# Optimization experiments

Measured on AMD Instinct MI355X. Metric: run time of the kernel, lower is better.

The kernel has to match this reference:

```python
import jax, jax.numpy as jnp
from jax import lax
import numpy as np

B, T, N, D = 16, 2048, 8, 512


def _div_term(d):
    # exp(arange(0,d,2) * -(ln 10000)/d), as in FixedEmbedding
    return jnp.exp(jnp.arange(0, d, 2).astype(jnp.float32) * (-np.log(10000.0) / d))


def _fixed_table(c, d):
    pos = jnp.arange(c, dtype=jnp.float32)[:, None]
    ang = pos * _div_term(d)  # [c, d/2]
    tab = jnp.zeros((c, d), dtype=jnp.float32)
    tab = tab.at[:, 0::2].set(jnp.sin(ang)).at[:, 1::2].set(jnp.cos(ang))
    return tab


def setup_inputs() -> dict:
    key = jax.random.key(0)
    k1, k2, k3 = jax.random.split(key, 3)
    x = jax.random.normal(k1, (B, T, N), dtype=jnp.float32)
    x_mark = jax.random.randint(k2, (B, T, 4), 0, 7).astype(jnp.int64)
    conv_w = jax.random.normal(k3, (D, N, 3), dtype=jnp.float32) * 0.05
    return {"x": x, "x_mark": x_mark, "conv_w": conv_w}


def reference(x, x_mark, conv_w):
    b, t, n = x.shape
    d = conv_w.shape[0]

    # --- TokenEmbedding: Conv1d(c_in->d_model, k=3, circular padding, no bias) ---
    xp = jnp.transpose(x, (0, 2, 1))  # [b, n, t]
    xpad = jnp.concatenate([xp[..., -1:], xp, xp[..., :1]], axis=-1)  # circular pad 1
    val = lax.conv_general_dilated(
        xpad, conv_w, window_strides=(1,), padding="VALID",
        dimension_numbers=("NCH", "OIH", "NCH"))  # [b, d, t]
    val = jnp.transpose(val, (0, 2, 1))  # [b, t, d]

    # --- TemporalEmbedding (fixed sinusoidal tables), freq='h' ---
    # columns: 0=month(<13), 1=day(<32), 2=weekday(<7), 3=hour(<24)
    temp = (_fixed_table(24, d)[x_mark[:, :, 3]]
            + _fixed_table(7, d)[x_mark[:, :, 2]]
            + _fixed_table(32, d)[x_mark[:, :, 1]]
            + _fixed_table(13, d)[x_mark[:, :, 0]])  # [b, t, d]

    # --- Cycle_PositionalEmbedding (k=1) ---
    fft_abs = jnp.abs(jnp.fft.rfft(x, axis=1))  # [b, t//2+1, n]
    top_idx = jnp.argmax(fft_abs, axis=1)  # [b, n]; topk(k=1) == argmax (first max)
    freqs = jnp.fft.fftfreq(t, d=1.0)  # length t; rfft indices are in range
    periods = jnp.clip(t / freqs[top_idx], 1.0, float(t))  # [b, n]; 0-freq -> inf -> t
    time_idx = jnp.arange(t, dtype=jnp.float32)[None, :, None]  # [1, t, 1]
    pidx = jnp.floor(time_idx % periods[:, None, :])  # [b, t, n] (.long() truncation)

    # FixedEmbedding row for index p is sin/cos(p*div) independent of c_in
    ang = pidx[..., None] * _div_term(d)  # [b, t, n, d/2]
    pe = jnp.stack([jnp.sin(ang), jnp.cos(ang)], axis=-1).reshape(b, t, n, d)
    cyc = pe.mean(axis=2)  # [b, t, d]

    # dropout is identity in eval mode
    return val + temp + cyc
```

## Files before the change

### kernel.cpp

```cpp
#include <hip/hip_runtime.h>
#include <math.h>

#define B_ 16
#define T_ 2048
#define N_ 8
#define D_ 512
#define DTW 4
#define LPAD 520

#define NEG_W0 (-3.0679615757712823e-3f)
#define NEG_W32 (-0.19634954084936207f)
#define NEG_W1024 (-6.1359231515425647e-3f)
#define NEG_LDIV (-0.035977892078031555f)

typedef __attribute__((ext_vector_type(8))) short bf16x8;
typedef __attribute__((ext_vector_type(4))) float f32x4;

static __device__ __forceinline__ short f2bf(float f) {
  unsigned int u = __float_as_uint(f);
  unsigned int r = u + 0x7FFFu + ((u >> 16) & 1u);
  return (short)(r >> 16);
}


__global__ __launch_bounds__(1024) void prep_kernel(
    const float* __restrict__ x, const int* __restrict__ xmark,
    const float* __restrict__ convw, float* __restrict__ pmax,
    float* __restrict__ nyqS, float* __restrict__ tab,
    short* __restrict__ amat, short* __restrict__ xbf,
    short* __restrict__ cnt) {
  int tid = threadIdx.x;
  int blk = blockIdx.x;

  if (blk >= 256) {
    int j = blk - 256;
    if (j < 32) {
      int r = j * 1024 + tid;
      const float4* xr = (const float4*)(x + (size_t)r * 8);
      float4 lo = xr[0], hi = xr[1];
      bf16x8 v;
      v[0] = f2bf(lo.x); v[1] = f2bf(lo.y); v[2] = f2bf(lo.z); v[3] = f2bf(lo.w);
      v[4] = f2bf(hi.x); v[5] = f2bf(hi.y); v[6] = f2bf(hi.z); v[7] = f2bf(hi.w);
      *(bf16x8*)(xbf + (size_t)r * 8) = v;
      int4 mk = *(const int4*)(xmark + (size_t)r * 4);
      bf16x8 cv;
#pragma unroll
      for (int p = 0; p < 8; ++p) {
        int cc = (mk.x == p) + (mk.y == p) + (mk.z == p) + (mk.w == p);
        cv[p] = f2bf((float)cc);
      }
      *(bf16x8*)(cnt + (size_t)r * 8) = cv;
    } else if (j == 32) {
      if (tid < 512) {
        int d = tid;
        short row[32];
#pragma unroll
        for (int kk = 0; kk < 24; ++kk) {
          int g = kk >> 3, n = kk & 7;
          row[kk] = f2bf(convw[d * 24 + n * 3 + g]);
        }
        float divv = expf((float)(d >> 1) * NEG_LDIV);
        float s1, c1;
        sincosf(divv, &s1, &c1);
        int odd = d & 1;
        row[24] = f2bf(odd ? 1.f : 0.f);
        float ps = s1, pc = c1;
        row[25] = f2bf(odd ? pc : ps);
#pragma unroll
        for (int p = 2; p < 7; ++p) {
          float ns = fmaf(ps, c1, pc * s1);
          float nc = fmaf(pc, c1, -ps * s1);
          ps = ns; pc = nc;
          row[24 + p] = f2bf(odd ? pc : ps);
        }
        row[31] = 0;
#pragma unroll
        for (int q = 0; q < 4; ++q)
          *(bf16x8*)(amat + d * 32 + q * 8) = *(bf16x8*)&row[q * 8];
      }
    } else {
      int gt = (j - 33) * 1024 + tid;
      int tb = gt >> 7;
      int d4 = gt & 127;
      float dv0 = expf((float)(d4 * 2) * NEG_LDIV);
      float dv1 = expf((float)(d4 * 2 + 1) * NEG_LDIV);
      float tf = (float)(tb * 16);
      float s0, c0, s1, c1, r0s, r0c, r1s, r1c;
      sincosf(tf * dv0, &s0, &c0);
      sincosf(tf * dv1, &s1, &c1);
      sincosf(dv0, &r0s, &r0c);
      sincosf(dv1, &r1s, &r1c);
      float* row = tab + (size_t)(tb * 16) * D_ + d4 * 4;
#pragma unroll
      for (int u = 0; u < 16; ++u) {
        f32x4 v; v[0] = s0; v[1] = c0; v[2] = s1; v[3] = c1;
        *(f32x4*)row = v;
        row += D_;
        float ns0 = fmaf(s0, r0c, c0 * r0s), nc0 = fmaf(c0, r0c, -s0 * r0s);
        s0 = ns0; c0 = nc0;
        float ns1 = fmaf(s1, r1c, c1 * r1s), nc1 = fmaf(c1, r1c, -s1 * r1s);
        s1 = ns1; c1 = nc1;
      }
    }
    return;
  }

  __shared__ __align__(16) float2 ybuf[1024];
  __shared__ __align__(16) float2 Bl[1024];
  __shared__ __align__(16) float2 part[1024];
  __shared__ float swav[16];
  __shared__ float pwav[8];
  int bn = blk >> 1, parity = blk & 1;
  int b = bn >> 3, n = bn & 7;
  const float* xb = x + (size_t)b * (T_ * N_) + n;

  float va = xb[tid * 8];
  float vb = xb[(tid + 1024) * 8];
  float ea = va + vb;
  float sgn = (tid & 1) ? -ea : ea;
#pragma unroll
  for (int off = 32; off > 0; off >>= 1) sgn += __shfl_down(sgn, off);
  if ((tid & 63) == 0) swav[tid >> 6] = sgn;

  if (parity == 0) {
    ((float*)ybuf)[tid] = ea;
  } else {
    float o = va - vb;
    float c0, s0;
    sincosf((float)tid * NEG_W0, &s0, &c0);
    ybuf[tid] = make_float2(o * c0, o * s0);
  }
  __syncthreads();

  int m0 = tid & 31, t0 = tid >> 5;
  float d1 = (float)m0 * NEG_W32;
  float K1 = 2.0f * cosf(d1);
  float c = 1.f, s = 0.f, cp, sp;
  sincosf(-d1, &sp, &cp);
  float ar = 0.f, ai = 0.f;
  if (parity == 0) {
    const float* ya = (const float*)ybuf;
#pragma unroll 8
    for (int t1 = 0; t1 < 32; ++t1) {
      float y = ya[t1 * 32 + t0];
      ar = fmaf(y, c, ar); ai = fmaf(y, s, ai);
      float nc = fmaf(K1, c, -cp), ns = fmaf(K1, s, -sp);
      cp = c; sp = s; c = nc; s = ns;
    }
  } else {
#pragma unroll 8
    for (int t1 = 0; t1 < 32; ++t1) {
      float2 y = ybuf[t1 * 32 + t0];
      ar = fmaf(y.x, c, fmaf(-y.y, s, ar));
      ai = fmaf(y.x, s, fmaf(y.y, c, ai));
      float nc = fmaf(K1, c, -cp), ns = fmaf(K1, s, -sp);
      cp = c; sp = s; c = nc; s = ns;
    }
  }
  {
    float ct, st;
    sincosf((float)(t0 * m0) * NEG_W1024, &st, &ct);
    Bl[t0 * 32 + m0] = make_float2(ar * ct - ai * st, fmaf(ar, st, ai * ct));
  }
  __syncthreads();

  int m02 = tid & 31;
  int m1 = (tid >> 5) & 15;
  int h = tid >> 9;
  float d2 = (float)m1 * NEG_W32;
  float K2 = 2.0f * cosf(d2);
  int t0s = h * 16;
  float c2, s2, c2p, s2p;
  sincosf((float)t0s * d2, &s2, &c2);
  sincosf((float)(t0s - 1) * d2, &s2p, &c2p);
  float yr = 0.f, yi = 0.f;
#pragma unroll 8
  for (int jj = 0; jj < 16; ++jj) {
    float2 bv = Bl[(t0s + jj) * 32 + m02];
    yr = fmaf(bv.x, c2, fmaf(-bv.y, s2, yr));
    yi = fmaf(bv.x, s2, fmaf(bv.y, c2, yi));
    float nc = fmaf(K2, c2, -c2p), ns = fmaf(K2, s2, -s2p);
    c2p = c2; s2p = s2; c2 = nc; s2 = ns;
  }
  part[tid] = make_float2(yr, yi);
  __syncthreads();
  if (tid < 512) {
    float2 pa = part[tid], pb = part[tid + 512];
    float rr = pa.x + pb.x, ii = pa.y + pb.y;
    float P = fmaf(rr, rr, ii * ii);
#pragma unroll
    for (int off = 32; off > 0; off >>= 1) P = fmaxf(P, __shfl_down(P, off));
    if ((tid & 63) == 0) pwav[tid >> 6] = P;
  }
  __syncthreads();
  if (tid < 64) {
    float mxv = (tid < 8) ? pwav[tid] : 0.f;
    float svv = (tid < 16) ? swav[tid] : 0.f;
#pragma unroll
    for (int off = 8; off > 0; off >>= 1) {
      mxv = fmaxf(mxv, __shfl_down(mxv, off));
      svv += __shfl_down(svv, off);
    }
    if (tid == 0) {
      pmax[blk] = mxv;
      if (parity == 0) nyqS[bn] = svv;
    }
  }
}

__global__ __launch_bounds__(512, 6) void main_kernel(
    const short* __restrict__ amat, const short* __restrict__ xbf,
    const short* __restrict__ cnt, const float* __restrict__ tab,
    const float* __restrict__ pmax, const float* __restrict__ nyqS,
    float* __restrict__ out) {
  __shared__ __align__(16) float lds[16 * LPAD];
  int tid = threadIdx.x;
  int lane = tid & 63;
  int w = tid >> 6;
  int c = lane & 15;
  int g = lane >> 4;
  int blk = blockIdx.x;
  int b = blk >> 7;
  int t0 = (blk & 127) * 16;

  int m = 0;
#pragma unroll
  for (int nn = 0; nn < 8; ++nn) {
    int bn = b * 8 + nn;
    float mx = fmaxf(pmax[2 * bn], pmax[2 * bn + 1]);
    float S = nyqS[bn];
    if (S * S > mx) ++m;
  }
  float w1 = (float)(8 - m) * 0.125f;
  float w0 = (float)m * 0.125f;

  bf16x8 afrag[DTW];
  f32x4 fet[DTW];
#pragma unroll
  for (int q = 0; q < DTW; ++q) {
    int d0 = (w * DTW + q) * 16;
    afrag[q] = *(const bf16x8*)(amat + (size_t)(d0 + c) * 32 + g * 8);
    fet[q] = *(const f32x4*)(tab + (size_t)(t0 + c) * D_ + d0 + g * 4);
  }

  bf16x8 bfrag;
  if (g < 3) {
    int row = (t0 + c + g - 1) & (T_ - 1);
    bfrag = *(const bf16x8*)(xbf + ((size_t)b * T_ + row) * 8);
  } else {
    bfrag = *(const bf16x8*)(cnt + ((size_t)b * T_ + t0 + c) * 8);
  }

  const f32x4 zac = {0.f, 0.f, 0.f, 0.f};
#pragma unroll
  for (int q = 0; q < DTW; ++q) {
    f32x4 acc = __builtin_amdgcn_mfma_f32_16x16x32_bf16(
        afrag[q], bfrag, zac, 0, 0, 0);
    f32x4 ov;
    ov[0] = fmaf(w1, fet[q][0], acc[0]);
    ov[1] = fmaf(w1, fet[q][1], acc[1]) + w0;
    ov[2] = fmaf(w1, fet[q][2], acc[2]);
    ov[3] = fmaf(w1, fet[q][3], acc[3]) + w0;
    int d0 = (w * DTW + q) * 16;
    *(f32x4*)(lds + c * LPAD + d0 + g * 4) = ov;
  }
  __syncthreads();
  float* obase = out + ((size_t)b * T_ + t0) * D_;
#pragma unroll
  for (int r = 0; r < 4; ++r) {
    int e = r * 2048 + tid * 4;
    int trow = e >> 9, col = e & 511;
    f32x4 v = *(const f32x4*)(lds + trow * LPAD + col);
    *(f32x4*)(obase + e) = v;
  }
}

extern "C" void kernel_launch(void* const* d_in, const int* in_sizes, int n_in,
                              void* d_out, int out_size, void* d_ws, size_t ws_size,
                              hipStream_t stream) {
  const float* x = (const float*)d_in[0];
  const int* xmark = (const int*)d_in[1];
  const float* convw = (const float*)d_in[2];
  float* out = (float*)d_out;

  char* ws = (char*)d_ws;
  float* pmax = (float*)ws;
  float* nyqS = pmax + 256;
  float* tab = (float*)(ws + 4096);
  short* amat = (short*)(ws + 4096 + 4194304);
  short* xbf = (short*)(ws + 4096 + 4194304 + 32768);
  short* cnt = (short*)(ws + 4096 + 4194304 + 32768 + 524288);

  prep_kernel<<<305, 1024, 0, stream>>>(x, xmark, convw, pmax, nyqS, tab,
                                        amat, xbf, cnt);
  main_kernel<<<B_ * (T_ / 16), 512, 0, stream>>>(amat, xbf, cnt, tab,
                                                  pmax, nyqS, out);
}
```

Baseline: 31.47 us.

## Reuse conv/table fragments across four batches per block and split FFT blocks

Measured after the change: 29.83 us. 1.06x faster.

```diff
diff --git a/kernel.cpp b/kernel.cpp
--- a/kernel.cpp
+++ b/kernel.cpp
@@ -23,7 +23,7 @@
 }
 
 
-__global__ __launch_bounds__(1024) void prep_kernel(
+__global__ __launch_bounds__(512) void prep_kernel(
     const float* __restrict__ x, const int* __restrict__ xmark,
     const float* __restrict__ convw, float* __restrict__ pmax,
     float* __restrict__ nyqS, float* __restrict__ tab,
@@ -32,10 +32,10 @@
   int tid = threadIdx.x;
   int blk = blockIdx.x;
 
-  if (blk >= 256) {
-    int j = blk - 256;
-    if (j < 32) {
-      int r = j * 1024 + tid;
+  if (blk >= 512) {
+    int j = blk - 512;
+    if (j < 64) {
+      int r = j * 512 + tid;
       const float4* xr = (const float4*)(x + (size_t)r * 8);
       float4 lo = xr[0], hi = xr[1];
       bf16x8 v;
@@ -50,36 +50,34 @@
         cv[p] = f2bf((float)cc);
       }
       *(bf16x8*)(cnt + (size_t)r * 8) = cv;
-    } else if (j == 32) {
-      if (tid < 512) {
-        int d = tid;
-        short row[32];
-#pragma unroll
-        for (int kk = 0; kk < 24; ++kk) {
-          int g = kk >> 3, n = kk & 7;
-          row[kk] = f2bf(convw[d * 24 + n * 3 + g]);
-        }
-        float divv = expf((float)(d >> 1) * NEG_LDIV);
-        float s1, c1;
-        sincosf(divv, &s1, &c1);
-        int odd = d & 1;
-        row[24] = f2bf(odd ? 1.f : 0.f);
-        float ps = s1, pc = c1;
-        row[25] = f2bf(odd ? pc : ps);
-#pragma unroll
-        for (int p = 2; p < 7; ++p) {
-          float ns = fmaf(ps, c1, pc * s1);
-          float nc = fmaf(pc, c1, -ps * s1);
-          ps = ns; pc = nc;
-          row[24 + p] = f2bf(odd ? pc : ps);
-        }
-        row[31] = 0;
-#pragma unroll
-        for (int q = 0; q < 4; ++q)
-          *(bf16x8*)(amat + d * 32 + q * 8) = *(bf16x8*)&row[q * 8];
+    } else if (j == 64) {
+      int d = tid;
+      short row[32];
+#pragma unroll
+      for (int kk = 0; kk < 24; ++kk) {
+        int g = kk >> 3, n = kk & 7;
+        row[kk] = f2bf(convw[d * 24 + n * 3 + g]);
       }
+      float divv = expf((float)(d >> 1) * NEG_LDIV);
+      float s1, c1;
+      sincosf(divv, &s1, &c1);
+      int odd = d & 1;
+      row[24] = f2bf(odd ? 1.f : 0.f);
+      float ps = s1, pc = c1;
+      row[25] = f2bf(odd ? pc : ps);
+#pragma unroll
+      for (int p = 2; p < 7; ++p) {
+        float ns = fmaf(ps, c1, pc * s1);
+        float nc = fmaf(pc, c1, -ps * s1);
+        ps = ns; pc = nc;
+        row[24 + p] = f2bf(odd ? pc : ps);
+      }
+      row[31] = 0;
+#pragma unroll
+      for (int q = 0; q < 4; ++q)
+        *(bf16x8*)(amat + d * 32 + q * 8) = *(bf16x8*)&row[q * 8];
     } else {
-      int gt = (j - 33) * 1024 + tid;
+      int gt = (j - 65) * 512 + tid;
       int tb = gt >> 7;
       int d4 = gt & 127;
       float dv0 = expf((float)(d4 * 2) * NEG_LDIV);
@@ -107,69 +105,86 @@
 
   __shared__ __align__(16) float2 ybuf[1024];
   __shared__ __align__(16) float2 Bl[1024];
-  __shared__ __align__(16) float2 part[1024];
-  __shared__ float swav[16];
-  __shared__ float pwav[8];
-  int bn = blk >> 1, parity = blk & 1;
+  __shared__ __align__(16) float2 part[512];
+  __shared__ float swav[8];
+  __shared__ float pwav[4];
+  int bn = blk >> 2;
+  int parity = (blk >> 1) & 1;
+  int h = blk & 1;
   int b = bn >> 3, n = bn & 7;
   const float* xb = x + (size_t)b * (T_ * N_) + n;
 
-  float va = xb[tid * 8];
-  float vb = xb[(tid + 1024) * 8];
-  float ea = va + vb;
-  float sgn = (tid & 1) ? -ea : ea;
+  float v0 = xb[tid * 8];
+  float v1 = xb[(tid + 512) * 8];
+  float v2 = xb[(tid + 1024) * 8];
+  float v3 = xb[(tid + 1536) * 8];
+  float ea = v0 + v2, eb = v1 + v3;
+  float sgn = (tid & 1) ? -(ea + eb) : (ea + eb);
 #pragma unroll
   for (int off = 32; off > 0; off >>= 1) sgn += __shfl_down(sgn, off);
   if ((tid & 63) == 0) swav[tid >> 6] = sgn;
 
   if (parity == 0) {
-    ((float*)ybuf)[tid] = ea;
+    float* ya = (float*)ybuf;
+    ya[tid] = ea;
+    ya[tid + 512] = eb;
   } else {
-    float o = va - vb;
-    float c0, s0;
-    sincosf((float)tid * NEG_W0, &s0, &c0);
-    ybuf[tid] = make_float2(o * c0, o * s0);
+    float oa = v0 - v2, ob = v1 - v3;
+    float ca, sa, cb, sb;
+    sincosf((float)tid * NEG_W0, &sa, &ca);
+    sincosf((float)(tid + 512) * NEG_W0, &sb, &cb);
+    ybuf[tid] = make_float2(oa * ca, oa * sa);
+    ybuf[tid + 512] = make_float2(ob * cb, ob * sb);
   }
   __syncthreads();
 
-  int m0 = tid & 31, t0 = tid >> 5;
+  int m0 = tid & 31, t0a = tid >> 5;
   float d1 = (float)m0 * NEG_W32;
   float K1 = 2.0f * cosf(d1);
   float c = 1.f, s = 0.f, cp, sp;
   sincosf(-d1, &sp, &cp);
-  float ar = 0.f, ai = 0.f;
+  float ar0 = 0.f, ai0 = 0.f, ar1 = 0.f, ai1 = 0.f;
   if (parity == 0) {
     const float* ya = (const float*)ybuf;
 #pragma unroll 8
     for (int t1 = 0; t1 < 32; ++t1) {
-      float y = ya[t1 * 32 + t0];
-      ar = fmaf(y, c, ar); ai = fmaf(y, s, ai);
+      float y0 = ya[t1 * 32 + t0a];
+      float y1 = ya[t1 * 32 + t0a + 16];
+      ar0 = fmaf(y0, c, ar0); ai0 = fmaf(y0, s, ai0);
+      ar1 = fmaf(y1, c, ar1); ai1 = fmaf(y1, s, ai1);
       float nc = fmaf(K1, c, -cp), ns = fmaf(K1, s, -sp);
       cp = c; sp = s; c = nc; s = ns;
     }
   } else {
 #pragma unroll 8
     for (int t1 = 0; t1 < 32; ++t1) {
-      float2 y = ybuf[t1 * 32 + t0];
-      ar = fmaf(y.x, c, fmaf(-y.y, s, ar));
-      ai = fmaf(y.x, s, fmaf(y.y, c, ai));
+      float2 y0 = ybuf[t1 * 32 + t0a];
+      float2 y1 = ybuf[t1 * 32 + t0a + 16];
+      ar0 = fmaf(y0.x, c, fmaf(-y0.y, s, ar0));
+      ai0 = fmaf(y0.x, s, fmaf(y0.y, c, ai0));
+      ar1 = fmaf(y1.x, c, fmaf(-y1.y, s, ar1));
+      ai1 = fmaf(y1.x, s, fmaf(y1.y, c, ai1));
       float nc = fmaf(K1, c, -cp), ns = fmaf(K1, s, -sp);
       cp = c; sp = s; c = nc; s = ns;
     }
   }
   {
     float ct, st;
-    sincosf((float)(t0 * m0) * NEG_W1024, &st, &ct);
-    Bl[t0 * 32 + m0] = make_float2(ar * ct - ai * st, fmaf(ar, st, ai * ct));
+    sincosf((float)(t0a * m0) * NEG_W1024, &st, &ct);
+    Bl[t0a * 32 + m0] =
+        make_float2(ar0 * ct - ai0 * st, fmaf(ar0, st, ai0 * ct));
+    sincosf((float)((t0a + 16) * m0) * NEG_W1024, &st, &ct);
+    Bl[(t0a + 16) * 32 + m0] =
+        make_float2(ar1 * ct - ai1 * st, fmaf(ar1, st, ai1 * ct));
   }
   __syncthreads();
 
   int m02 = tid & 31;
-  int m1 = (tid >> 5) & 15;
-  int h = tid >> 9;
+  int m1 = h * 8 + ((tid >> 5) & 7);
+  int th = tid >> 8;
   float d2 = (float)m1 * NEG_W32;
   float K2 = 2.0f * cosf(d2);
-  int t0s = h * 16;
+  int t0s = th * 16;
   float c2, s2, c2p, s2p;
   sincosf((float)t0s * d2, &s2, &c2);
   sincosf((float)(t0s - 1) * d2, &s2p, &c2p);
@@ -184,8 +199,8 @@
   }
   part[tid] = make_float2(yr, yi);
   __syncthreads();
-  if (tid < 512) {
-    float2 pa = part[tid], pb = part[tid + 512];
+  if (tid < 256) {
+    float2 pa = part[tid], pb = part[tid + 256];
     float rr = pa.x + pb.x, ii = pa.y + pb.y;
     float P = fmaf(rr, rr, ii * ii);
 #pragma unroll
@@ -194,10 +209,10 @@
   }
   __syncthreads();
   if (tid < 64) {
-    float mxv = (tid < 8) ? pwav[tid] : 0.f;
-    float svv = (tid < 16) ? swav[tid] : 0.f;
-#pragma unroll
-    for (int off = 8; off > 0; off >>= 1) {
+    float mxv = (tid < 4) ? pwav[tid] : 0.f;
+    float svv = (tid < 8) ? swav[tid] : 0.f;
+#pragma unroll
+    for (int off = 4; off > 0; off >>= 1) {
       mxv = fmaxf(mxv, __shfl_down(mxv, off));
       svv += __shfl_down(svv, off);
     }
@@ -208,7 +223,7 @@
   }
 }
 
-__global__ __launch_bounds__(512, 6) void main_kernel(
+__global__ __launch_bounds__(512, 4) void main_kernel(
     const short* __restrict__ amat, const short* __restrict__ xbf,
     const short* __restrict__ cnt, const float* __restrict__ tab,
     const float* __restrict__ pmax, const float* __restrict__ nyqS,
@@ -220,19 +235,26 @@
   int c = lane & 15;
   int g = lane >> 4;
   int blk = blockIdx.x;
-  int b = blk >> 7;
-  int t0 = (blk & 127) * 16;
-
-  int m = 0;
-#pragma unroll
-  for (int nn = 0; nn < 8; ++nn) {
-    int bn = b * 8 + nn;
-    float mx = fmaxf(pmax[2 * bn], pmax[2 * bn + 1]);
-    float S = nyqS[bn];
-    if (S * S > mx) ++m;
-  }
-  float w1 = (float)(8 - m) * 0.125f;
-  float w0 = (float)m * 0.125f;
+  int ttile = blk >> 2;
+  int bg = blk & 3;
+  int t0 = ttile * 16;
+
+  float w1v[4], w0v[4];
+#pragma unroll
+  for (int j = 0; j < 4; ++j) {
+    int b = bg * 4 + j;
+    int m = 0;
+#pragma unroll
+    for (int nn = 0; nn < 8; ++nn) {
+      int bn = b * 8 + nn;
+      float mx = fmaxf(fmaxf(pmax[4 * bn], pmax[4 * bn + 1]),
+                       fmaxf(pmax[4 * bn + 2], pmax[4 * bn + 3]));
+      float S = nyqS[bn];
+      if (S * S > mx) ++m;
+    }
+    w1v[j] = (float)(8 - m) * 0.125f;
+    w0v[j] = (float)m * 0.125f;
+  }
 
   bf16x8 afrag[DTW];
   f32x4 fet[DTW];
@@ -243,35 +265,40 @@
     fet[q] = *(const f32x4*)(tab + (size_t)(t0 + c) * D_ + d0 + g * 4);
   }
 
-  bf16x8 bfrag;
-  if (g < 3) {
-    int row = (t0 + c + g - 1) & (T_ - 1);
-    bfrag = *(const bf16x8*)(xbf + ((size_t)b * T_ + row) * 8);
-  } else {
-    bfrag = *(const bf16x8*)(cnt + ((size_t)b * T_ + t0 + c) * 8);
-  }
-
   const f32x4 zac = {0.f, 0.f, 0.f, 0.f};
 #pragma unroll
-  for (int q = 0; q < DTW; ++q) {
-    f32x4 acc = __builtin_amdgcn_mfma_f32_16x16x32_bf16(
-        afrag[q], bfrag, zac, 0, 0, 0);
-    f32x4 ov;
-    ov[0] = fmaf(w1, fet[q][0], acc[0]);
-    ov[1] = fmaf(w1, fet[q][1], acc[1]) + w0;
-    ov[2] = fmaf(w1, fet[q][2], acc[2]);
-    ov[3] = fmaf(w1, fet[q][3], acc[3]) + w0;
-    int d0 = (w * DTW + q) * 16;
-    *(f32x4*)(lds + c * LPAD + d0 + g * 4) = ov;
-  }
-  __syncthreads();
-  float* obase = out + ((size_t)b * T_ + t0) * D_;
-#pragma unroll
-  for (int r = 0; r < 4; ++r) {
-    int e = r * 2048 + tid * 4;
-    int trow = e >> 9, col = e & 511;
-    f32x4 v = *(const f32x4*)(lds + trow * LPAD + col);
-    *(f32x4*)(obase + e) = v;
+  for (int j = 0; j < 4; ++j) {
+    int b = bg * 4 + j;
+    bf16x8 bfrag;
+    if (g < 3) {
+      int row = (t0 + c + g - 1) & (T_ - 1);
+      bfrag = *(const bf16x8*)(xbf + ((size_t)b * T_ + row) * 8);
+    } else {
+      bfrag = *(const bf16x8*)(cnt + ((size_t)b * T_ + t0 + c) * 8);
+    }
+    float w1 = w1v[j], w0 = w0v[j];
+#pragma unroll
+    for (int q = 0; q < DTW; ++q) {
+      f32x4 acc = __builtin_amdgcn_mfma_f32_16x16x32_bf16(
+          afrag[q], bfrag, zac, 0, 0, 0);
+      f32x4 ov;
+      ov[0] = fmaf(w1, fet[q][0], acc[0]);
+      ov[1] = fmaf(w1, fet[q][1], acc[1]) + w0;
+      ov[2] = fmaf(w1, fet[q][2], acc[2]);
+      ov[3] = fmaf(w1, fet[q][3], acc[3]) + w0;
+      int d0 = (w * DTW + q) * 16;
+      *(f32x4*)(lds + c * LPAD + d0 + g * 4) = ov;
+    }
+    __syncthreads();
+    float* obase = out + ((size_t)b * T_ + t0) * D_;
+#pragma unroll
+    for (int r = 0; r < 4; ++r) {
+      int e = r * 2048 + tid * 4;
+      int trow = e >> 9, col = e & 511;
+      f32x4 v = *(const f32x4*)(lds + trow * LPAD + col);
+      *(f32x4*)(obase + e) = v;
+    }
+    __syncthreads();
   }
 }
 
@@ -285,14 +312,14 @@
 
   char* ws = (char*)d_ws;
   float* pmax = (float*)ws;
-  float* nyqS = pmax + 256;
+  float* nyqS = pmax + 512;
   float* tab = (float*)(ws + 4096);
   short* amat = (short*)(ws + 4096 + 4194304);
   short* xbf = (short*)(ws + 4096 + 4194304 + 32768);
   short* cnt = (short*)(ws + 4096 + 4194304 + 32768 + 524288);
 
-  prep_kernel<<<305, 1024, 0, stream>>>(x, xmark, convw, pmax, nyqS, tab,
-                                        amat, xbf, cnt);
-  main_kernel<<<B_ * (T_ / 16), 512, 0, stream>>>(amat, xbf, cnt, tab,
-                                                  pmax, nyqS, out);
+  prep_kernel<<<609, 512, 0, stream>>>(x, xmark, convw, pmax, nyqS, tab,
+                                       amat, xbf, cnt);
+  main_kernel<<<(T_ / 16) * (B_ / 4), 512, 0, stream>>>(amat, xbf, cnt, tab,
+                                                        pmax, nyqS, out);
 }
```

## Split DFT over 4x more small blocks and process two batches per main block

Applied to the files above, without the earlier changes.

Measured after the change: 34.67 us. 10.2% more time.

```diff
diff --git a/kernel.cpp b/kernel.cpp
--- a/kernel.cpp
+++ b/kernel.cpp
@@ -23,7 +23,7 @@
 }
 
 
-__global__ __launch_bounds__(1024) void prep_kernel(
+__global__ __launch_bounds__(256) void prep_kernel(
     const float* __restrict__ x, const int* __restrict__ xmark,
     const float* __restrict__ convw, float* __restrict__ pmax,
     float* __restrict__ nyqS, float* __restrict__ tab,
@@ -32,54 +32,10 @@
   int tid = threadIdx.x;
   int blk = blockIdx.x;
 
-  if (blk >= 256) {
-    int j = blk - 256;
-    if (j < 32) {
-      int r = j * 1024 + tid;
-      const float4* xr = (const float4*)(x + (size_t)r * 8);
-      float4 lo = xr[0], hi = xr[1];
-      bf16x8 v;
-      v[0] = f2bf(lo.x); v[1] = f2bf(lo.y); v[2] = f2bf(lo.z); v[3] = f2bf(lo.w);
-      v[4] = f2bf(hi.x); v[5] = f2bf(hi.y); v[6] = f2bf(hi.z); v[7] = f2bf(hi.w);
-      *(bf16x8*)(xbf + (size_t)r * 8) = v;
-      int4 mk = *(const int4*)(xmark + (size_t)r * 4);
-      bf16x8 cv;
-#pragma unroll
-      for (int p = 0; p < 8; ++p) {
-        int cc = (mk.x == p) + (mk.y == p) + (mk.z == p) + (mk.w == p);
-        cv[p] = f2bf((float)cc);
-      }
-      *(bf16x8*)(cnt + (size_t)r * 8) = cv;
-    } else if (j == 32) {
-      if (tid < 512) {
-        int d = tid;
-        short row[32];
-#pragma unroll
-        for (int kk = 0; kk < 24; ++kk) {
-          int g = kk >> 3, n = kk & 7;
-          row[kk] = f2bf(convw[d * 24 + n * 3 + g]);
-        }
-        float divv = expf((float)(d >> 1) * NEG_LDIV);
-        float s1, c1;
-        sincosf(divv, &s1, &c1);
-        int odd = d & 1;
-        row[24] = f2bf(odd ? 1.f : 0.f);
-        float ps = s1, pc = c1;
-        row[25] = f2bf(odd ? pc : ps);
-#pragma unroll
-        for (int p = 2; p < 7; ++p) {
-          float ns = fmaf(ps, c1, pc * s1);
-          float nc = fmaf(pc, c1, -ps * s1);
-          ps = ns; pc = nc;
-          row[24 + p] = f2bf(odd ? pc : ps);
-        }
-        row[31] = 0;
-#pragma unroll
-        for (int q = 0; q < 4; ++q)
-          *(bf16x8*)(amat + d * 32 + q * 8) = *(bf16x8*)&row[q * 8];
-      }
-    } else {
-      int gt = (j - 33) * 1024 + tid;
+  if (blk >= 1024) {
+    int j = blk - 1024;
+    if (j < 64) {
+      int gt = j * 256 + tid;
       int tb = gt >> 7;
       int d4 = gt & 127;
       float dv0 = expf((float)(d4 * 2) * NEG_LDIV);
@@ -101,75 +57,146 @@
         float ns1 = fmaf(s1, r1c, c1 * r1s), nc1 = fmaf(c1, r1c, -s1 * r1s);
         s1 = ns1; c1 = nc1;
       }
+    } else if (j < 192) {
+      int r = (j - 64) * 256 + tid;
+      const float4* xr = (const float4*)(x + (size_t)r * 8);
+      float4 lo = xr[0], hi = xr[1];
+      bf16x8 v;
+      v[0] = f2bf(lo.x); v[1] = f2bf(lo.y); v[2] = f2bf(lo.z); v[3] = f2bf(lo.w);
+      v[4] = f2bf(hi.x); v[5] = f2bf(hi.y); v[6] = f2bf(hi.z); v[7] = f2bf(hi.w);
+      *(bf16x8*)(xbf + (size_t)r * 8) = v;
+      int4 mk = *(const int4*)(xmark + (size_t)r * 4);
+      bf16x8 cv;
+#pragma unroll
+      for (int p = 0; p < 8; ++p) {
+        int cc = (mk.x == p) + (mk.y == p) + (mk.z == p) + (mk.w == p);
+        cv[p] = f2bf((float)cc);
+      }
+      *(bf16x8*)(cnt + (size_t)r * 8) = cv;
+    } else {
+      int d = (j - 192) * 256 + tid;
+      short row[32];
+#pragma unroll
+      for (int kk = 0; kk < 24; ++kk) {
+        int g = kk >> 3, n = kk & 7;
+        row[kk] = f2bf(convw[d * 24 + n * 3 + g]);
+      }
+      float divv = expf((float)(d >> 1) * NEG_LDIV);
+      float s1, c1;
+      sincosf(divv, &s1, &c1);
+      int odd = d & 1;
+      row[24] = f2bf(odd ? 1.f : 0.f);
+      float ps = s1, pc = c1;
+      row[25] = f2bf(odd ? pc : ps);
+#pragma unroll
+      for (int p = 2; p < 7; ++p) {
+        float ns = fmaf(ps, c1, pc * s1);
+        float nc = fmaf(pc, c1, -ps * s1);
+        ps = ns; pc = nc;
+        row[24 + p] = f2bf(odd ? pc : ps);
+      }
+      row[31] = 0;
+#pragma unroll
+      for (int q = 0; q < 4; ++q)
+        *(bf16x8*)(amat + d * 32 + q * 8) = *(bf16x8*)&row[q * 8];
     }
     return;
   }
 
   __shared__ __align__(16) float2 ybuf[1024];
   __shared__ __align__(16) float2 Bl[1024];
-  __shared__ __align__(16) float2 part[1024];
-  __shared__ float swav[16];
-  __shared__ float pwav[8];
-  int bn = blk >> 1, parity = blk & 1;
+  __shared__ __align__(16) float2 part[256];
+  __shared__ float swav[4];
+  __shared__ float pwav[2];
+  int bn = blk >> 3;
+  int parity = (blk >> 2) & 1;
+  int h = blk & 3;
   int b = bn >> 3, n = bn & 7;
   const float* xb = x + (size_t)b * (T_ * N_) + n;
 
-  float va = xb[tid * 8];
-  float vb = xb[(tid + 1024) * 8];
-  float ea = va + vb;
-  float sgn = (tid & 1) ? -ea : ea;
+  float ev[4], ov[4];
+  float esum = 0.f;
+#pragma unroll
+  for (int j = 0; j < 4; ++j) {
+    int t = tid + j * 256;
+    float va = xb[t * 8];
+    float vb = xb[(t + 1024) * 8];
+    ev[j] = va + vb;
+    ov[j] = va - vb;
+    esum += ev[j];
+  }
+  float sgn = (tid & 1) ? -esum : esum;
 #pragma unroll
   for (int off = 32; off > 0; off >>= 1) sgn += __shfl_down(sgn, off);
   if ((tid & 63) == 0) swav[tid >> 6] = sgn;
 
   if (parity == 0) {
-    ((float*)ybuf)[tid] = ea;
+    float* ya = (float*)ybuf;
+#pragma unroll
+    for (int j = 0; j < 4; ++j) ya[tid + j * 256] = ev[j];
   } else {
-    float o = va - vb;
-    float c0, s0;
-    sincosf((float)tid * NEG_W0, &s0, &c0);
-    ybuf[tid] = make_float2(o * c0, o * s0);
+#pragma unroll
+    for (int j = 0; j < 4; ++j) {
+      int t = tid + j * 256;
+      float c0, s0;
+      sincosf((float)t * NEG_W0, &s0, &c0);
+      ybuf[t] = make_float2(ov[j] * c0, ov[j] * s0);
+    }
   }
   __syncthreads();
 
-  int m0 = tid & 31, t0 = tid >> 5;
+  int m0 = tid & 31, t0g = tid >> 5;
   float d1 = (float)m0 * NEG_W32;
   float K1 = 2.0f * cosf(d1);
   float c = 1.f, s = 0.f, cp, sp;
   sincosf(-d1, &sp, &cp);
-  float ar = 0.f, ai = 0.f;
+  float ar[4] = {0.f, 0.f, 0.f, 0.f}, ai[4] = {0.f, 0.f, 0.f, 0.f};
   if (parity == 0) {
-    const float* ya = (const float*)ybuf;
+    const float4* ya4 = (const float4*)ybuf;
 #pragma unroll 8
     for (int t1 = 0; t1 < 32; ++t1) {
-      float y = ya[t1 * 32 + t0];
-      ar = fmaf(y, c, ar); ai = fmaf(y, s, ai);
+      float4 y = ya4[t1 * 8 + t0g];
+      ar[0] = fmaf(y.x, c, ar[0]); ai[0] = fmaf(y.x, s, ai[0]);
+      ar[1] = fmaf(y.y, c, ar[1]); ai[1] = fmaf(y.y, s, ai[1]);
+      ar[2] = fmaf(y.z, c, ar[2]); ai[2] = fmaf(y.z, s, ai[2]);
+      ar[3] = fmaf(y.w, c, ar[3]); ai[3] = fmaf(y.w, s, ai[3]);
       float nc = fmaf(K1, c, -cp), ns = fmaf(K1, s, -sp);
       cp = c; sp = s; c = nc; s = ns;
     }
   } else {
+    const float4* yb4 = (const float4*)ybuf;
 #pragma unroll 8
     for (int t1 = 0; t1 < 32; ++t1) {
-      float2 y = ybuf[t1 * 32 + t0];
-      ar = fmaf(y.x, c, fmaf(-y.y, s, ar));
-      ai = fmaf(y.x, s, fmaf(y.y, c, ai));
+      float4 p0 = yb4[t1 * 16 + t0g * 2];
+      float4 p1 = yb4[t1 * 16 + t0g * 2 + 1];
+      ar[0] = fmaf(p0.x, c, fmaf(-p0.y, s, ar[0]));
+      ai[0] = fmaf(p0.x, s, fmaf(p0.y, c, ai[0]));
+      ar[1] = fmaf(p0.z, c, fmaf(-p0.w, s, ar[1]));
+      ai[1] = fmaf(p0.z, s, fmaf(p0.w, c, ai[1]));
+      ar[2] = fmaf(p1.x, c, fmaf(-p1.y, s, ar[2]));
+      ai[2] = fmaf(p1.x, s, fmaf(p1.y, c, ai[2]));
+      ar[3] = fmaf(p1.z, c, fmaf(-p1.w, s, ar[3]));
+      ai[3] = fmaf(p1.z, s, fmaf(p1.w, c, ai[3]));
       float nc = fmaf(K1, c, -cp), ns = fmaf(K1, s, -sp);
       cp = c; sp = s; c = nc; s = ns;
     }
   }
-  {
+#pragma unroll
+  for (int j = 0; j < 4; ++j) {
+    int t0 = t0g * 4 + j;
     float ct, st;
     sincosf((float)(t0 * m0) * NEG_W1024, &st, &ct);
-    Bl[t0 * 32 + m0] = make_float2(ar * ct - ai * st, fmaf(ar, st, ai * ct));
+    Bl[t0 * 32 + m0] =
+        make_float2(ar[j] * ct - ai[j] * st, fmaf(ar[j], st, ai[j] * ct));
   }
   __syncthreads();
 
   int m02 = tid & 31;
-  int m1 = (tid >> 5) & 15;
-  int h = tid >> 9;
+  int m1 = h * 4 + ((tid >> 5) & 3);
+  int th = tid >> 7;
   float d2 = (float)m1 * NEG_W32;
   float K2 = 2.0f * cosf(d2);
-  int t0s = h * 16;
+  int t0s = th * 16;
   float c2, s2, c2p, s2p;
   sincosf((float)t0s * d2, &s2, &c2);
   sincosf((float)(t0s - 1) * d2, &s2p, &c2p);
@@ -184,8 +211,8 @@
   }
   part[tid] = make_float2(yr, yi);
   __syncthreads();
-  if (tid < 512) {
-    float2 pa = part[tid], pb = part[tid + 512];
+  if (tid < 128) {
+    float2 pa = part[tid], pb = part[tid + 128];
     float rr = pa.x + pb.x, ii = pa.y + pb.y;
     float P = fmaf(rr, rr, ii * ii);
 #pragma unroll
@@ -193,18 +220,10 @@
     if ((tid & 63) == 0) pwav[tid >> 6] = P;
   }
   __syncthreads();
-  if (tid < 64) {
-    float mxv = (tid < 8) ? pwav[tid] : 0.f;
-    float svv = (tid < 16) ? swav[tid] : 0.f;
-#pragma unroll
-    for (int off = 8; off > 0; off >>= 1) {
-      mxv = fmaxf(mxv, __shfl_down(mxv, off));
-      svv += __shfl_down(svv, off);
-    }
-    if (tid == 0) {
-      pmax[blk] = mxv;
-      if (parity == 0) nyqS[bn] = svv;
-    }
+  if (tid == 0) {
+    pmax[blk] = fmaxf(pwav[0], pwav[1]);
+    if (parity == 0 && h == 0)
+      nyqS[bn] = swav[0] + swav[1] + swav[2] + swav[3];
   }
 }
 
@@ -220,19 +239,27 @@
   int c = lane & 15;
   int g = lane >> 4;
   int blk = blockIdx.x;
-  int b = blk >> 7;
-  int t0 = (blk & 127) * 16;
-
-  int m = 0;
-#pragma unroll
-  for (int nn = 0; nn < 8; ++nn) {
-    int bn = b * 8 + nn;
-    float mx = fmaxf(pmax[2 * bn], pmax[2 * bn + 1]);
-    float S = nyqS[bn];
-    if (S * S > mx) ++m;
-  }
-  float w1 = (float)(8 - m) * 0.125f;
-  float w0 = (float)m * 0.125f;
+  int ttile = blk & 127;
+  int bg = blk >> 7;
+  int t0 = ttile * 16;
+
+  float w1v[2], w0v[2];
+#pragma unroll
+  for (int j = 0; j < 2; ++j) {
+    int b = bg * 2 + j;
+    int m = 0;
+#pragma unroll
+    for (int nn = 0; nn < 8; ++nn) {
+      int bn = b * 8 + nn;
+      float mx = 0.f;
+#pragma unroll
+      for (int k = 0; k < 8; ++k) mx = fmaxf(mx, pmax[8 * bn + k]);
+      float S = nyqS[bn];
+      if (S * S > mx) ++m;
+    }
+    w1v[j] = (float)(8 - m) * 0.125f;
+    w0v[j] = (float)m * 0.125f;
+  }
 
   bf16x8 afrag[DTW];
   f32x4 fet[DTW];
@@ -243,35 +270,40 @@
     fet[q] = *(const f32x4*)(tab + (size_t)(t0 + c) * D_ + d0 + g * 4);
   }
 
-  bf16x8 bfrag;
-  if (g < 3) {
-    int row = (t0 + c + g - 1) & (T_ - 1);
-    bfrag = *(const bf16x8*)(xbf + ((size_t)b * T_ + row) * 8);
-  } else {
-    bfrag = *(const bf16x8*)(cnt + ((size_t)b * T_ + t0 + c) * 8);
-  }
-
   const f32x4 zac = {0.f, 0.f, 0.f, 0.f};
 #pragma unroll
-  for (int q = 0; q < DTW; ++q) {
-    f32x4 acc = __builtin_amdgcn_mfma_f32_16x16x32_bf16(
-        afrag[q], bfrag, zac, 0, 0, 0);
-    f32x4 ov;
-    ov[0] = fmaf(w1, fet[q][0], acc[0]);
-    ov[1] = fmaf(w1, fet[q][1], acc[1]) + w0;
-    ov[2] = fmaf(w1, fet[q][2], acc[2]);
-    ov[3] = fmaf(w1, fet[q][3], acc[3]) + w0;
-    int d0 = (w * DTW + q) * 16;
-    *(f32x4*)(lds + c * LPAD + d0 + g * 4) = ov;
-  }
-  __syncthreads();
-  float* obase = out + ((size_t)b * T_ + t0) * D_;
-#pragma unroll
-  for (int r = 0; r < 4; ++r) {
-    int e = r * 2048 + tid * 4;
-    int trow = e >> 9, col = e & 511;
-    f32x4 v = *(const f32x4*)(lds + trow * LPAD + col);
-    *(f32x4*)(obase + e) = v;
+  for (int j = 0; j < 2; ++j) {
+    int b = bg * 2 + j;
+    bf16x8 bfrag;
+    if (g < 3) {
+      int row = (t0 + c + g - 1) & (T_ - 1);
+      bfrag = *(const bf16x8*)(xbf + ((size_t)b * T_ + row) * 8);
+    } else {
+      bfrag = *(const bf16x8*)(cnt + ((size_t)b * T_ + t0 + c) * 8);
+    }
+    float w1 = w1v[j], w0 = w0v[j];
+#pragma unroll
+    for (int q = 0; q < DTW; ++q) {
+      f32x4 acc = __builtin_amdgcn_mfma_f32_16x16x32_bf16(
+          afrag[q], bfrag, zac, 0, 0, 0);
+      f32x4 ov;
+      ov[0] = fmaf(w1, fet[q][0], acc[0]);
+      ov[1] = fmaf(w1, fet[q][1], acc[1]) + w0;
+      ov[2] = fmaf(w1, fet[q][2], acc[2]);
+      ov[3] = fmaf(w1, fet[q][3], acc[3]) + w0;
+      int d0 = (w * DTW + q) * 16;
+      *(f32x4*)(lds + c * LPAD + d0 + g * 4) = ov;
+    }
+    __syncthreads();
+    float* obase = out + ((size_t)b * T_ + t0) * D_;
+#pragma unroll
+    for (int r = 0; r < 4; ++r) {
+      int e = r * 2048 + tid * 4;
+      int trow = e >> 9, col = e & 511;
+      f32x4 v = *(const f32x4*)(lds + trow * LPAD + col);
+      *(f32x4*)(obase + e) = v;
+    }
+    if (j == 0) __syncthreads();
   }
 }
 
@@ -285,14 +317,14 @@
 
   char* ws = (char*)d_ws;
   float* pmax = (float*)ws;
-  float* nyqS = pmax + 256;
-  float* tab = (float*)(ws + 4096);
-  short* amat = (short*)(ws + 4096 + 4194304);
-  short* xbf = (short*)(ws + 4096 + 4194304 + 32768);
-  short* cnt = (short*)(ws + 4096 + 4194304 + 32768 + 524288);
-
-  prep_kernel<<<305, 1024, 0, stream>>>(x, xmark, convw, pmax, nyqS, tab,
+  float* nyqS = pmax + 1024;
+  float* tab = (float*)(ws + 8192);
+  short* amat = (short*)(ws + 8192 + 4194304);
+  short* xbf = (short*)(ws + 8192 + 4194304 + 32768);
+  short* cnt = (short*)(ws + 8192 + 4194304 + 32768 + 524288);
+
+  prep_kernel<<<1218, 256, 0, stream>>>(x, xmark, convw, pmax, nyqS, tab,
                                         amat, xbf, cnt);
-  main_kernel<<<B_ * (T_ / 16), 512, 0, stream>>>(amat, xbf, cnt, tab,
-                                                  pmax, nyqS, out);
+  main_kernel<<<(T_ / 16) * (B_ / 2), 512, 0, stream>>>(amat, xbf, cnt, tab,
+                                                        pmax, nyqS, out);
 }
```
